# Optimization experiments

Measured on AMD Instinct MI355X. Metric: run time of the kernel, lower is better.

Reference implementation:

```python
import jax, jax.numpy as jnp
import numpy as np

B, SQ, SK = 32, 512, 512
Q_DIM = 512
K_DIM = 512
H = 8
HD = 64
INNER = H * HD
MAX_POS = 512
SCALE = 1.0 / np.sqrt(HD)


def setup_inputs() -> dict:
    key = jax.random.key(0)
    ks = jax.random.split(key, 10)
    query = jax.random.normal(ks[0], (B, SQ, Q_DIM), dtype=jnp.float32)
    key_t = jax.random.normal(ks[1], (B, SK, K_DIM), dtype=jnp.float32)
    value = jax.random.normal(ks[2], (B, SK, K_DIM), dtype=jnp.float32)
    mask = jax.random.randint(ks[3], (B, SQ, SK), 0, 2, dtype=jnp.int32)
    # learned parameters (Linear weights stored as [in, out]; to_q/k/v have no bias)
    Wq = jax.random.normal(ks[4], (Q_DIM, INNER), dtype=jnp.float32) * 0.02
    Wk = jax.random.normal(ks[5], (K_DIM, INNER), dtype=jnp.float32) * 0.02
    Wv = jax.random.normal(ks[6], (K_DIM, INNER), dtype=jnp.float32) * 0.02
    Wo = jax.random.normal(ks[7], (INNER, Q_DIM), dtype=jnp.float32) * 0.02
    bo = jnp.zeros((Q_DIM,), dtype=jnp.float32)
    rel_pos_emb = jax.random.normal(ks[8], (MAX_POS, MAX_POS), dtype=jnp.float32) * 0.02
    return {"query": query, "key": key_t, "value": value, "mask": mask,
            "Wq": Wq, "Wk": Wk, "Wv": Wv, "Wo": Wo, "bo": bo,
            "rel_pos_emb": rel_pos_emb}


def reference(query, key, value, mask, Wq, Wk, Wv, Wo, bo, rel_pos_emb):
    # Projections (no bias for q/k/v)
    q = query @ Wq   # [B, SQ, INNER]
    k = key @ Wk     # [B, SK, INNER]
    v = value @ Wv   # [B, SK, INNER]
    # split heads -> [B, H, S, HD]
    q = q.reshape(B, SQ, H, HD).transpose(0, 2, 1, 3)
    k = k.reshape(B, SK, H, HD).transpose(0, 2, 1, 3)
    v = v.reshape(B, SK, H, HD).transpose(0, 2, 1, 3)
    # scaled scores + learned relative-position bias (shared across batch/heads)
    scores = jnp.einsum('bhqd,bhkd->bhqk', q, k) * SCALE
    bias = rel_pos_emb[:SQ, :SK]          # [SQ, SK]
    scores = scores + bias[None, None, :, :]
    # additive masking: positions where mask == 0 get -inf
    scores = jnp.where(mask[:, None, :, :] == 0, -jnp.inf, scores)
    attn = jax.nn.softmax(scores, axis=-1)
    # dropout is identity in eval mode (p treated as inference)
    out = jnp.einsum('bhqk,bhkd->bhqd', attn, v)
    out = out.transpose(0, 2, 1, 3).reshape(B, SQ, INNER)
    return out @ Wo + bo
```

## Files before the change

### kernel.cpp

```cpp
#include <hip/hip_runtime.h>
#include <stdint.h>


typedef unsigned short u16;
typedef __attribute__((ext_vector_type(4))) float f32x4;
typedef __attribute__((ext_vector_type(8))) __bf16 bf16x8;
typedef __attribute__((ext_vector_type(4))) unsigned short u16x4;
typedef __attribute__((ext_vector_type(8))) unsigned short u16x8;
typedef __attribute__((ext_vector_type(4))) int i32x4;
typedef __attribute__((ext_vector_type(4))) _Float16 f16x4;
typedef __attribute__((ext_vector_type(8))) _Float16 f16x8;

#define MFMA16(a, b, c) __builtin_amdgcn_mfma_f32_16x16x32_bf16((a), (b), (c), 0, 0, 0)

#define LGKM0_BARRIER()                                        \
  do {                                                         \
    asm volatile("s_waitcnt lgkmcnt(0)" ::: "memory");         \
    __builtin_amdgcn_s_barrier();                              \
    __builtin_amdgcn_sched_barrier(0);                         \
  } while (0)

__device__ __forceinline__ u16 f2bf(float f) {
  unsigned u = __float_as_uint(f);
  u += 0x7fffu + ((u >> 16) & 1u);
  return (u16)(u >> 16);
}
__device__ __forceinline__ float bf2f(u16 h) {
  return __uint_as_float(((unsigned)h) << 16);
}

__device__ __forceinline__ void gl_lds16(const void* g, void* l) {
  __builtin_amdgcn_global_load_lds(
      (const __attribute__((address_space(1))) unsigned int*)g,
      (__attribute__((address_space(3))) unsigned int*)l, 16, 0, 0);
}

__global__ __launch_bounds__(256) void k_prep(
    const float* __restrict__ Wq, const float* __restrict__ Wk,
    const float* __restrict__ Wv, const float* __restrict__ Wo,
    u16* __restrict__ Wt, u16* __restrict__ WoHi, u16* __restrict__ WoLo) {
  int idx = blockIdx.x * 256 + threadIdx.x;
  int n = idx >> 9, k = idx & 511;
  int src = k * 512 + n;
  Wt[idx]          = f2bf(Wq[src]);
  Wt[262144 + idx] = f2bf(Wk[src]);
  Wt[524288 + idx] = f2bf(Wv[src]);
  float wo = Wo[src];
  u16 hi = f2bf(wo);
  WoHi[idx] = hi;
  WoLo[idx] = f2bf(wo - bf2f(hi));
}

__global__ __launch_bounds__(256) void k_cvt(
    const float* __restrict__ Xq, const float* __restrict__ Xk,
    const float* __restrict__ Xv, u16* __restrict__ Xb) {
  const float* __restrict__ src =
      (blockIdx.y == 0) ? Xq : (blockIdx.y == 1) ? Xk : Xv;
  size_t i8 = ((size_t)blockIdx.x * 256 + threadIdx.x) * 8;
  f32x4 v0 = *(const f32x4*)&src[i8];
  f32x4 v1 = *(const f32x4*)&src[i8 + 4];
  u16x8 o;
#pragma unroll
  for (int e = 0; e < 4; ++e) {
    o[e]     = f2bf(v0[e]);
    o[e + 4] = f2bf(v1[e]);
  }
  *(u16x8*)&Xb[(size_t)blockIdx.y * 8388608 + i8] = o;
}

__global__ __launch_bounds__(256) void k_mb(
    const int* __restrict__ mask, const float* __restrict__ bias,
    _Float16* __restrict__ MB) {
  size_t i8 = ((size_t)blockIdx.x * 256 + threadIdx.x) * 8;
  i32x4 m0 = *(const i32x4*)&mask[i8];
  i32x4 m1 = *(const i32x4*)&mask[i8 + 4];
  size_t bi = i8 & 262143;
  f32x4 b0 = *(const f32x4*)&bias[bi];
  f32x4 b1 = *(const f32x4*)&bias[bi + 4];
  const _Float16 MASKED = (_Float16)(-60000.0f);
  f16x8 o;
#pragma unroll
  for (int e = 0; e < 4; ++e) {
    o[e]     = (m0[e] != 0) ? (_Float16)b0[e] : MASKED;
    o[e + 4] = (m1[e] != 0) ? (_Float16)b1[e] : MASKED;
  }
  *(f16x8*)&MB[i8] = o;
}

__global__ __launch_bounds__(512, 4) void k_proj(
    const u16* __restrict__ Xb, const u16* __restrict__ Wt,
    u16* __restrict__ Qb, u16* __restrict__ Kb, u16* __restrict__ Vtb) {
  __shared__ __align__(16) u16 lAb[2][128][64];
  const int mat = blockIdx.z;
  const u16* __restrict__ Ab = Xb + (size_t)mat * 8388608;
  const u16* __restrict__ Bw = Wt + (size_t)mat * 262144;
  const int tid = threadIdx.x, lane = tid & 63, wid = tid >> 6;
  const int wm = wid >> 2, wn = wid & 3;
  const int m0 = blockIdx.y * 128, n0 = blockIdx.x * 256;
  const int fr = lane & 15, g = lane >> 4;

  const int sub = lane >> 3;
  const int xo = ((lane & 7) ^ sub) * 8;
  const int swr = (fr & 7) << 4;

  const u16* __restrict__ Bp[4];
#pragma unroll
  for (int fn = 0; fn < 4; ++fn)
    Bp[fn] = &Bw[(size_t)(n0 + wn * 64 + fn * 16 + fr) * 512 + g * 8];

  f32x4 acc[4][4] = {};

#pragma unroll
  for (int p = 0; p < 2; ++p) {
    const int rb = p * 64 + wid * 8;
    gl_lds16(Ab + (size_t)(m0 + rb + sub) * 512 + xo, &lAb[0][rb][0]);
  }
  __syncthreads();

  for (int kt = 0; kt < 8; ++kt) {
    const int cur = kt & 1, nxt = cur ^ 1;
    const int k0 = kt * 64;
    bf16x8 bB[2][4];
#pragma unroll
    for (int fn = 0; fn < 4; ++fn) {
      bB[0][fn] = *(const bf16x8*)(Bp[fn] + k0);
      bB[1][fn] = *(const bf16x8*)(Bp[fn] + k0 + 32);
    }
    if (kt < 7) {
#pragma unroll
      for (int p = 0; p < 2; ++p) {
        const int rb = p * 64 + wid * 8;
        gl_lds16(Ab + (size_t)(m0 + rb + sub) * 512 + k0 + 64 + xo,
                 &lAb[nxt][rb][0]);
      }
    }
#pragma unroll
    for (int kc = 0; kc < 2; ++kc) {
#pragma unroll
      for (int fm = 0; fm < 4; ++fm) {
        const char* rowb = (const char*)&lAb[cur][wm * 64 + fm * 16 + fr][0];
        bf16x8 af = *(const bf16x8*)(rowb + ((kc * 64 + g * 16) ^ swr));
#pragma unroll
        for (int fn = 0; fn < 4; ++fn)
          acc[fm][fn] = MFMA16(af, bB[kc][fn], acc[fm][fn]);
      }
    }
    __syncthreads();
  }

  if (mat < 2) {
    u16* __restrict__ Out = (mat == 0) ? Qb : Kb;
#pragma unroll
    for (int fm = 0; fm < 4; ++fm) {
#pragma unroll
      for (int fn = 0; fn < 4; ++fn) {
        int gn = n0 + wn * 64 + fn * 16 + fr;
        int hh = gn >> 6, hd = gn & 63;
#pragma unroll
        for (int r = 0; r < 4; ++r) {
          int gm = m0 + wm * 64 + fm * 16 + g * 4 + r;
          int b = gm >> 9, sq = gm & 511;
          Out[(size_t)((b * 8 + hh) * 512 + sq) * 64 + hd] = f2bf(acc[fm][fn][r]);
        }
      }
    }
  } else {
#pragma unroll
    for (int fm = 0; fm < 4; ++fm) {
      int gm0 = m0 + wm * 64 + fm * 16 + g * 4;
      int b = gm0 >> 9, sq0 = gm0 & 511;
#pragma unroll
      for (int fn = 0; fn < 4; ++fn) {
        int gn = n0 + wn * 64 + fn * 16 + fr;
        int hh = gn >> 6, hd = gn & 63;
        u16x4 pv;
        pv[0] = f2bf(acc[fm][fn][0]); pv[1] = f2bf(acc[fm][fn][1]);
        pv[2] = f2bf(acc[fm][fn][2]); pv[3] = f2bf(acc[fm][fn][3]);
        *(u16x4*)&Vtb[(size_t)((b * 8 + hh) * 64 + hd) * 512 + sq0] = pv;
      }
    }
  }
}

__global__ __launch_bounds__(256, 4) void k_attn(
    const u16* __restrict__ Qb, const u16* __restrict__ Kb, const u16* __restrict__ Vtb,
    const _Float16* __restrict__ MB, float* __restrict__ Obuf) {
  __shared__ __align__(16) u16 kbuf[2][64][64];
  __shared__ __align__(16) u16 vbuf[2][64][64];
  __shared__ __align__(16) u16 lP[4][16][64];
  const int tid = threadIdx.x, lane = tid & 63, w = tid >> 6;
  const int orig = blockIdx.x;
  const int xcd = orig & 7, idx = orig >> 3;
  const int qq = idx & 3, h = (idx >> 2) & 7;
  const int b = xcd + 8 * (idx >> 5);
  const int bh = b * 8 + h;
  const int fr = lane & 15, g = lane >> 4;
  const int sq0 = qq * 128 + w * 32;
  const int sw = (fr & 7) << 4;
  const u16* __restrict__ Qh = Qb + (size_t)bh * 32768;
  const u16* __restrict__ Kh = Kb + (size_t)bh * 32768;
  const u16* __restrict__ Vh = Vtb + (size_t)bh * 32768;
  const _Float16* __restrict__ MBr = MB + (size_t)b * 262144 + (size_t)(sq0 + fr) * 512;
  char* lProw = (char*)&lP[w][fr][0];
  const char* kcb;
  const char* vcb;

  const int sub = lane >> 3;
  const int xo = ((lane & 7) ^ sub) * 8;

  bf16x8 qf[2][2];
#pragma unroll
  for (int qfi = 0; qfi < 2; ++qfi)
#pragma unroll
    for (int kc = 0; kc < 2; ++kc)
      qf[qfi][kc] = *(const bf16x8*)&Qh[(size_t)(sq0 + qfi * 16 + fr) * 64 + kc * 32 + g * 8];

  f32x4 oacc[2][4] = {};
  float mrow[2] = {-1e30f, -1e30f}, lrow[2] = {0.f, 0.f};

  {
    if (w < 2) {
      const int rb = w * 32;
      const u16* gs = Kh + (size_t)(rb + sub) * 64 + xo;
#pragma unroll
      for (int i = 0; i < 4; ++i)
        gl_lds16(gs + (size_t)i * 8 * 64, &kbuf[0][rb + i * 8][0]);
    } else {
      const int rb = (w - 2) * 32;
      const u16* gs = Vh + (size_t)(rb + sub) * 512 + xo;
#pragma unroll
      for (int i = 0; i < 4; ++i)
        gl_lds16(gs + (size_t)i * 8 * 512, &vbuf[0][rb + i * 8][0]);
    }
  }
  __syncthreads();

  int cur = 0;
  for (int kt = 0; kt < 8; ++kt) {
    const int sk0 = kt * 64;
    f16x4 mbv[2][4];
#pragma unroll
    for (int qfi = 0; qfi < 2; ++qfi)
#pragma unroll
      for (int fn = 0; fn < 4; ++fn)
        mbv[qfi][fn] = *(const f16x4*)&MBr[(size_t)qfi * 16 * 512 + sk0 + fn * 16 + g * 4];
    if (kt < 7) {
      const int nb = cur ^ 1, sk0n = sk0 + 64;
      if (w < 2) {
        const int rb = w * 32;
        const u16* gs = Kh + (size_t)(sk0n + rb + sub) * 64 + xo;
#pragma unroll
        for (int i = 0; i < 4; ++i)
          gl_lds16(gs + (size_t)i * 8 * 64, &kbuf[nb][rb + i * 8][0]);
      } else {
        const int rb = (w - 2) * 32;
        const u16* gs = Vh + (size_t)(rb + sub) * 512 + sk0n + xo;
#pragma unroll
        for (int i = 0; i < 4; ++i)
          gl_lds16(gs + (size_t)i * 8 * 512, &vbuf[nb][rb + i * 8][0]);
      }
    }
    kcb = (const char*)kbuf[cur];
    vcb = (const char*)vbuf[cur];
    f32x4 sacc[2][4] = {};
#pragma unroll
    for (int fn = 0; fn < 4; ++fn) {
      const int r = fn * 16 + fr;
      bf16x8 kf0 = *(const bf16x8*)(kcb + (size_t)r * 128 + ((0 * 64 + g * 16) ^ sw));
      bf16x8 kf1 = *(const bf16x8*)(kcb + (size_t)r * 128 + ((1 * 64 + g * 16) ^ sw));
      sacc[0][fn] = MFMA16(kf0, qf[0][0], sacc[0][fn]);
      sacc[0][fn] = MFMA16(kf1, qf[0][1], sacc[0][fn]);
      sacc[1][fn] = MFMA16(kf0, qf[1][0], sacc[1][fn]);
      sacc[1][fn] = MFMA16(kf1, qf[1][1], sacc[1][fn]);
    }
#pragma unroll
    for (int qfi = 0; qfi < 2; ++qfi)
#pragma unroll
      for (int fn = 0; fn < 4; ++fn)
#pragma unroll
        for (int r = 0; r < 4; ++r)
          sacc[qfi][fn][r] = sacc[qfi][fn][r] * 0.125f + (float)mbv[qfi][fn][r];

#pragma unroll
    for (int qfi = 0; qfi < 2; ++qfi) {
      float t0 = fmaxf(fmaxf(sacc[qfi][0][0], sacc[qfi][0][1]),
                       fmaxf(sacc[qfi][0][2], sacc[qfi][0][3]));
      float t1 = fmaxf(fmaxf(sacc[qfi][1][0], sacc[qfi][1][1]),
                       fmaxf(sacc[qfi][1][2], sacc[qfi][1][3]));
      float t2 = fmaxf(fmaxf(sacc[qfi][2][0], sacc[qfi][2][1]),
                       fmaxf(sacc[qfi][2][2], sacc[qfi][2][3]));
      float t3 = fmaxf(fmaxf(sacc[qfi][3][0], sacc[qfi][3][1]),
                       fmaxf(sacc[qfi][3][2], sacc[qfi][3][3]));
      float pm = fmaxf(fmaxf(t0, t1), fmaxf(t2, t3));
      pm = fmaxf(pm, __shfl_xor(pm, 16));
      pm = fmaxf(pm, __shfl_xor(pm, 32));
      if (!__all(pm - mrow[qfi] <= 8.0f)) {
        float mn = fmaxf(mrow[qfi], pm);
        float sfac = __expf(mrow[qfi] - mn);
        mrow[qfi] = mn;
        lrow[qfi] *= sfac;
#pragma unroll
        for (int r = 0; r < 4; ++r) {
          float sr = __shfl(sfac, g * 4 + r);
#pragma unroll
          for (int fnh = 0; fnh < 4; ++fnh)
            oacc[qfi][fnh][r] *= sr;
        }
      }
      float ps = 0.f;
#pragma unroll
      for (int fn = 0; fn < 4; ++fn) {
        float p0 = __expf(sacc[qfi][fn][0] - mrow[qfi]);
        float p1 = __expf(sacc[qfi][fn][1] - mrow[qfi]);
        float p2 = __expf(sacc[qfi][fn][2] - mrow[qfi]);
        float p3 = __expf(sacc[qfi][fn][3] - mrow[qfi]);
        ps += (p0 + p1) + (p2 + p3);
        u16x4 pw;
        pw[0] = f2bf(p0); pw[1] = f2bf(p1); pw[2] = f2bf(p2); pw[3] = f2bf(p3);
        *(u16x4*)(lProw + ((fn * 32 + g * 8) ^ sw)) = pw;
      }
      ps += __shfl_xor(ps, 16);
      ps += __shfl_xor(ps, 32);
      lrow[qfi] += ps;
      __builtin_amdgcn_wave_barrier();
#pragma unroll
      for (int kc = 0; kc < 2; ++kc) {
        bf16x8 pf = *(const bf16x8*)(lProw + ((kc * 64 + g * 16) ^ sw));
#pragma unroll
        for (int fnh = 0; fnh < 4; ++fnh) {
          const int vr = fnh * 16 + fr;
          bf16x8 vf = *(const bf16x8*)(vcb + (size_t)vr * 128 + ((kc * 64 + g * 16) ^ sw));
          oacc[qfi][fnh] = MFMA16(pf, vf, oacc[qfi][fnh]);
        }
      }
      __builtin_amdgcn_wave_barrier();
    }
    __syncthreads();
    cur ^= 1;
  }
#pragma unroll
  for (int qfi = 0; qfi < 2; ++qfi) {
#pragma unroll
    for (int r = 0; r < 4; ++r) {
      float lr = __shfl(lrow[qfi], g * 4 + r);
      float inv = 1.0f / lr;
      const int sq = sq0 + qfi * 16 + g * 4 + r;
      float* orow = &Obuf[((size_t)b * 512 + sq) * 512 + h * 64];
#pragma unroll
      for (int fnh = 0; fnh < 4; ++fnh)
        orow[fnh * 16 + fr] = oacc[qfi][fnh][r] * inv;
    }
  }
}

__global__ __launch_bounds__(512, 4) void k_out(
    const float* __restrict__ Oin, const u16* __restrict__ WoHi, const u16* __restrict__ WoLo,
    const float* __restrict__ bo, float* __restrict__ out) {
  __shared__ __align__(16) u16 lAh[2][64][40], lAl[2][64][40];
  const int tid = threadIdx.x, lane = tid & 63, wn = tid >> 6;
  const int m0 = blockIdx.y * 64, n0 = blockIdx.x * 256;
  const int fr = lane & 15, g = lane >> 4;
  const int arow = tid >> 3, acg = tid & 7;
  const float* __restrict__ Ar = &Oin[(size_t)(m0 + arow) * 512 + acg * 4];
  const u16* __restrict__ Bh[2];
  const u16* __restrict__ Bl[2];
#pragma unroll
  for (int fn = 0; fn < 2; ++fn) {
    size_t row = (size_t)(n0 + wn * 32 + fn * 16 + fr) * 512 + g * 8;
    Bh[fn] = &WoHi[row];
    Bl[fn] = &WoLo[row];
  }

  f32x4 acc[4][2] = {};
  f32x4 va[2];

  {
    f32x4 v = *(const f32x4*)&Ar[0];
    va[0] = *(const f32x4*)&Ar[32];
    u16x4 hv, lv;
#pragma unroll
    for (int e = 0; e < 4; ++e) {
      u16 hb = f2bf(v[e]);
      hv[e] = hb;
      lv[e] = f2bf(v[e] - bf2f(hb));
    }
    *(u16x4*)&lAh[0][arow][acg * 4] = hv;
    *(u16x4*)&lAl[0][arow][acg * 4] = lv;
  }
  LGKM0_BARRIER();

#pragma unroll
  for (int kt = 0; kt < 16; ++kt) {
    const int cur = kt & 1, nxt = cur ^ 1;
    const int k0 = kt * 32;
    bf16x8 bh[2], bl[2];
#pragma unroll
    for (int fn = 0; fn < 2; ++fn) {
      bh[fn] = *(const bf16x8*)(Bh[fn] + k0);
      bl[fn] = *(const bf16x8*)(Bl[fn] + k0);
    }
    if (kt < 14)
      va[nxt] = *(const f32x4*)&Ar[(kt + 2) * 32];
#pragma unroll
    for (int fm = 0; fm < 4; ++fm) {
      bf16x8 ah = *(const bf16x8*)&lAh[cur][fm * 16 + fr][g * 8];
      bf16x8 al = *(const bf16x8*)&lAl[cur][fm * 16 + fr][g * 8];
#pragma unroll
      for (int fn = 0; fn < 2; ++fn) {
        acc[fm][fn] = MFMA16(ah, bh[fn], acc[fm][fn]);
        acc[fm][fn] = MFMA16(ah, bl[fn], acc[fm][fn]);
        acc[fm][fn] = MFMA16(al, bh[fn], acc[fm][fn]);
      }
    }
    if (kt < 15) {
      u16x4 hv, lv;
#pragma unroll
      for (int e = 0; e < 4; ++e) {
        u16 hb = f2bf(va[cur][e]);
        hv[e] = hb;
        lv[e] = f2bf(va[cur][e] - bf2f(hb));
      }
      *(u16x4*)&lAh[nxt][arow][acg * 4] = hv;
      *(u16x4*)&lAl[nxt][arow][acg * 4] = lv;
    }
    LGKM0_BARRIER();
  }

#pragma unroll
  for (int fm = 0; fm < 4; ++fm) {
#pragma unroll
    for (int fn = 0; fn < 2; ++fn) {
      int gn = n0 + wn * 32 + fn * 16 + fr;
      float bv = bo[gn];
#pragma unroll
      for (int r = 0; r < 4; ++r) {
        int gm = m0 + fm * 16 + g * 4 + r;
        out[(size_t)gm * 512 + gn] = acc[fm][fn][r] + bv;
      }
    }
  }
}

extern "C" void kernel_launch(void* const* d_in, const int* in_sizes, int n_in,
                              void* d_out, int out_size, void* d_ws, size_t ws_size,
                              hipStream_t stream) {
  (void)in_sizes; (void)n_in; (void)out_size; (void)ws_size;
  const float* query = (const float*)d_in[0];
  const float* key_t = (const float*)d_in[1];
  const float* value = (const float*)d_in[2];
  const int*   mask  = (const int*)d_in[3];
  const float* Wq    = (const float*)d_in[4];
  const float* Wk    = (const float*)d_in[5];
  const float* Wv    = (const float*)d_in[6];
  const float* Wo    = (const float*)d_in[7];
  const float* bo    = (const float*)d_in[8];
  const float* bias  = (const float*)d_in[9];
  float* out = (float*)d_out;

  char* p = (char*)d_ws;
  u16* Wt   = (u16*)p; p += (size_t)3 * 512 * 512 * 2;
  u16* WoHi = (u16*)p; p += (size_t)512 * 512 * 2;
  u16* WoLo = (u16*)p; p += (size_t)512 * 512 * 2;
  u16* Qb   = (u16*)p; p += (size_t)32 * 8 * 512 * 64 * 2;
  u16* Kb   = (u16*)p; p += (size_t)32 * 8 * 512 * 64 * 2;
  u16* Vtb  = (u16*)p; p += (size_t)32 * 8 * 512 * 64 * 2;
  u16* Xb = (u16*)p;
  float* Obuf = (float*)p;
  _Float16* MBp = (_Float16*)(p + (size_t)32 * 512 * 512 * 4);

  k_prep<<<1024, 256, 0, stream>>>(Wq, Wk, Wv, Wo, Wt, WoHi, WoLo);
  k_cvt<<<dim3(4096, 3), 256, 0, stream>>>(query, key_t, value, Xb);
  k_proj<<<dim3(2, 128, 3), 512, 0, stream>>>(Xb, Wt, Qb, Kb, Vtb);
  k_mb<<<4096, 256, 0, stream>>>(mask, bias, MBp);
  k_attn<<<1024, 256, 0, stream>>>(Qb, Kb, Vtb, MBp, Obuf);
  k_out<<<dim3(2, 256), 512, 0, stream>>>(Obuf, WoHi, WoLo, bo, out);
}
```

Measured before the change: 194.3 us.

## Pre-swizzle weights into MFMA fragment order and shrink proj/out blocks to 256 threads

The weight prep kernel now writes Wq/Wk/Wv and the Wo hi/lo split in MFMA B-fragment order. Each wave can then load its B operand as one fully contiguous 1KB chunk per k-step instead of strided row reads. k_proj and k_out are reshaped to 256-thread blocks covering 128 output columns, with twice as many blocks launched and A-tile loading adjusted to match. This targets uncoalesced weight loads and aims at better occupancy, at the cost of reloading A tiles across more column blocks.

```diff
diff --git a/kernel.cpp b/kernel.cpp
--- a/kernel.cpp
+++ b/kernel.cpp
@@ -39,16 +39,32 @@
     const float* __restrict__ Wq, const float* __restrict__ Wk,
     const float* __restrict__ Wv, const float* __restrict__ Wo,
     u16* __restrict__ Wt, u16* __restrict__ WoHi, u16* __restrict__ WoLo) {
-  int idx = blockIdx.x * 256 + threadIdx.x;
-  int n = idx >> 9, k = idx & 511;
-  int src = k * 512 + n;
-  Wt[idx]          = f2bf(Wq[src]);
-  Wt[262144 + idx] = f2bf(Wk[src]);
-  Wt[524288 + idx] = f2bf(Wv[src]);
-  float wo = Wo[src];
-  u16 hi = f2bf(wo);
-  WoHi[idx] = hi;
-  WoLo[idx] = f2bf(wo - bf2f(hi));
+  int t = blockIdx.x * 256 + threadIdx.x;
+  int mat = t >> 15;
+  int r = t & 32767;
+  int nc = r >> 10, kb = (r >> 6) & 15, lane = r & 63;
+  int fr = lane & 15, g = lane >> 4;
+  int n = nc * 16 + fr;
+  int kbase = kb * 32 + g * 8;
+  if (mat < 3) {
+    const float* __restrict__ W = (mat == 0) ? Wq : (mat == 1) ? Wk : Wv;
+    u16x8 o;
+#pragma unroll
+    for (int j = 0; j < 8; ++j)
+      o[j] = f2bf(W[(size_t)(kbase + j) * 512 + n]);
+    *(u16x8*)&Wt[(size_t)mat * 262144 + (size_t)r * 8] = o;
+  } else {
+    u16x8 oh, ol;
+#pragma unroll
+    for (int j = 0; j < 8; ++j) {
+      float wo = Wo[(size_t)(kbase + j) * 512 + n];
+      u16 hi = f2bf(wo);
+      oh[j] = hi;
+      ol[j] = f2bf(wo - bf2f(hi));
+    }
+    *(u16x8*)&WoHi[(size_t)r * 8] = oh;
+    *(u16x8*)&WoLo[(size_t)r * 8] = ol;
+  }
 }
 
 __global__ __launch_bounds__(256) void k_cvt(
@@ -87,32 +103,33 @@
   *(f16x8*)&MB[i8] = o;
 }
 
-__global__ __launch_bounds__(512, 4) void k_proj(
+__global__ __launch_bounds__(256, 4) void k_proj(
     const u16* __restrict__ Xb, const u16* __restrict__ Wt,
     u16* __restrict__ Qb, u16* __restrict__ Kb, u16* __restrict__ Vtb) {
   __shared__ __align__(16) u16 lAb[2][128][64];
   const int mat = blockIdx.z;
   const u16* __restrict__ Ab = Xb + (size_t)mat * 8388608;
-  const u16* __restrict__ Bw = Wt + (size_t)mat * 262144;
+  const u16* __restrict__ Bf = Wt + (size_t)mat * 262144;
   const int tid = threadIdx.x, lane = tid & 63, wid = tid >> 6;
-  const int wm = wid >> 2, wn = wid & 3;
-  const int m0 = blockIdx.y * 128, n0 = blockIdx.x * 256;
+  const int wm = wid >> 1, wn = wid & 1;
+  const int m0 = blockIdx.y * 128, n0 = blockIdx.x * 128;
   const int fr = lane & 15, g = lane >> 4;
 
   const int sub = lane >> 3;
   const int xo = ((lane & 7) ^ sub) * 8;
   const int swr = (fr & 7) << 4;
 
-  const u16* __restrict__ Bp[4];
+  const int nc0 = (n0 >> 4) + wn * 4;
+  const u16* __restrict__ Bq[4];
 #pragma unroll
   for (int fn = 0; fn < 4; ++fn)
-    Bp[fn] = &Bw[(size_t)(n0 + wn * 64 + fn * 16 + fr) * 512 + g * 8];
+    Bq[fn] = Bf + (size_t)((nc0 + fn) * 16) * 512 + lane * 8;
 
   f32x4 acc[4][4] = {};
 
 #pragma unroll
-  for (int p = 0; p < 2; ++p) {
-    const int rb = p * 64 + wid * 8;
+  for (int p = 0; p < 4; ++p) {
+    const int rb = p * 32 + wid * 8;
     gl_lds16(Ab + (size_t)(m0 + rb + sub) * 512 + xo, &lAb[0][rb][0]);
   }
   __syncthreads();
@@ -123,13 +140,13 @@
     bf16x8 bB[2][4];
 #pragma unroll
     for (int fn = 0; fn < 4; ++fn) {
-      bB[0][fn] = *(const bf16x8*)(Bp[fn] + k0);
-      bB[1][fn] = *(const bf16x8*)(Bp[fn] + k0 + 32);
+      bB[0][fn] = *(const bf16x8*)(Bq[fn] + (size_t)(kt * 2) * 512);
+      bB[1][fn] = *(const bf16x8*)(Bq[fn] + (size_t)(kt * 2 + 1) * 512);
     }
     if (kt < 7) {
 #pragma unroll
-      for (int p = 0; p < 2; ++p) {
-        const int rb = p * 64 + wid * 8;
+      for (int p = 0; p < 4; ++p) {
+        const int rb = p * 32 + wid * 8;
         gl_lds16(Ab + (size_t)(m0 + rb + sub) * 512 + k0 + 64 + xo,
                  &lAb[nxt][rb][0]);
       }
@@ -353,54 +370,60 @@
   }
 }
 
-__global__ __launch_bounds__(512, 4) void k_out(
+__global__ __launch_bounds__(256, 4) void k_out(
     const float* __restrict__ Oin, const u16* __restrict__ WoHi, const u16* __restrict__ WoLo,
     const float* __restrict__ bo, float* __restrict__ out) {
   __shared__ __align__(16) u16 lAh[2][64][40], lAl[2][64][40];
   const int tid = threadIdx.x, lane = tid & 63, wn = tid >> 6;
-  const int m0 = blockIdx.y * 64, n0 = blockIdx.x * 256;
+  const int m0 = blockIdx.y * 64, n0 = blockIdx.x * 128;
   const int fr = lane & 15, g = lane >> 4;
-  const int arow = tid >> 3, acg = tid & 7;
-  const float* __restrict__ Ar = &Oin[(size_t)(m0 + arow) * 512 + acg * 4];
-  const u16* __restrict__ Bh[2];
-  const u16* __restrict__ Bl[2];
+  const int arow = tid >> 2, acg = tid & 3;
+  const float* __restrict__ Ar = &Oin[(size_t)(m0 + arow) * 512 + acg * 8];
+  const int nc0 = (n0 >> 4) + wn * 2;
+  const u16* __restrict__ Bhp[2];
+  const u16* __restrict__ Blp[2];
 #pragma unroll
   for (int fn = 0; fn < 2; ++fn) {
-    size_t row = (size_t)(n0 + wn * 32 + fn * 16 + fr) * 512 + g * 8;
-    Bh[fn] = &WoHi[row];
-    Bl[fn] = &WoLo[row];
+    size_t off = (size_t)((nc0 + fn) * 16) * 512 + lane * 8;
+    Bhp[fn] = WoHi + off;
+    Blp[fn] = WoLo + off;
   }
 
   f32x4 acc[4][2] = {};
-  f32x4 va[2];
+  f32x4 va[2][2];
 
   {
-    f32x4 v = *(const f32x4*)&Ar[0];
-    va[0] = *(const f32x4*)&Ar[32];
-    u16x4 hv, lv;
+    f32x4 v0 = *(const f32x4*)&Ar[0];
+    f32x4 v1 = *(const f32x4*)&Ar[4];
+    va[0][0] = *(const f32x4*)&Ar[32];
+    va[0][1] = *(const f32x4*)&Ar[36];
+    u16x8 hv, lv;
 #pragma unroll
     for (int e = 0; e < 4; ++e) {
-      u16 hb = f2bf(v[e]);
-      hv[e] = hb;
-      lv[e] = f2bf(v[e] - bf2f(hb));
-    }
-    *(u16x4*)&lAh[0][arow][acg * 4] = hv;
-    *(u16x4*)&lAl[0][arow][acg * 4] = lv;
+      u16 hb0 = f2bf(v0[e]);
+      u16 hb1 = f2bf(v1[e]);
+      hv[e] = hb0; hv[e + 4] = hb1;
+      lv[e] = f2bf(v0[e] - bf2f(hb0));
+      lv[e + 4] = f2bf(v1[e] - bf2f(hb1));
+    }
+    *(u16x8*)&lAh[0][arow][acg * 8] = hv;
+    *(u16x8*)&lAl[0][arow][acg * 8] = lv;
   }
   LGKM0_BARRIER();
 
 #pragma unroll
   for (int kt = 0; kt < 16; ++kt) {
     const int cur = kt & 1, nxt = cur ^ 1;
-    const int k0 = kt * 32;
     bf16x8 bh[2], bl[2];
 #pragma unroll
     for (int fn = 0; fn < 2; ++fn) {
-      bh[fn] = *(const bf16x8*)(Bh[fn] + k0);
-      bl[fn] = *(const bf16x8*)(Bl[fn] + k0);
-    }
-    if (kt < 14)
-      va[nxt] = *(const f32x4*)&Ar[(kt + 2) * 32];
+      bh[fn] = *(const bf16x8*)(Bhp[fn] + (size_t)kt * 512);
+      bl[fn] = *(const bf16x8*)(Blp[fn] + (size_t)kt * 512);
+    }
+    if (kt < 14) {
+      va[nxt][0] = *(const f32x4*)&Ar[(kt + 2) * 32];
+      va[nxt][1] = *(const f32x4*)&Ar[(kt + 2) * 32 + 4];
+    }
 #pragma unroll
     for (int fm = 0; fm < 4; ++fm) {
       bf16x8 ah = *(const bf16x8*)&lAh[cur][fm * 16 + fr][g * 8];
@@ -413,15 +436,17 @@
       }
     }
     if (kt < 15) {
-      u16x4 hv, lv;
+      u16x8 hv, lv;
 #pragma unroll
       for (int e = 0; e < 4; ++e) {
-        u16 hb = f2bf(va[cur][e]);
-        hv[e] = hb;
-        lv[e] = f2bf(va[cur][e] - bf2f(hb));
-      }
-      *(u16x4*)&lAh[nxt][arow][acg * 4] = hv;
-      *(u16x4*)&lAl[nxt][arow][acg * 4] = lv;
+        u16 hb0 = f2bf(va[cur][0][e]);
+        u16 hb1 = f2bf(va[cur][1][e]);
+        hv[e] = hb0; hv[e + 4] = hb1;
+        lv[e] = f2bf(va[cur][0][e] - bf2f(hb0));
+        lv[e + 4] = f2bf(va[cur][1][e] - bf2f(hb1));
+      }
+      *(u16x8*)&lAh[nxt][arow][acg * 8] = hv;
+      *(u16x8*)&lAl[nxt][arow][acg * 8] = lv;
     }
     LGKM0_BARRIER();
   }
@@ -468,10 +493,10 @@
   float* Obuf = (float*)p;
   _Float16* MBp = (_Float16*)(p + (size_t)32 * 512 * 512 * 4);
 
-  k_prep<<<1024, 256, 0, stream>>>(Wq, Wk, Wv, Wo, Wt, WoHi, WoLo);
+  k_prep<<<512, 256, 0, stream>>>(Wq, Wk, Wv, Wo, Wt, WoHi, WoLo);
   k_cvt<<<dim3(4096, 3), 256, 0, stream>>>(query, key_t, value, Xb);
-  k_proj<<<dim3(2, 128, 3), 512, 0, stream>>>(Xb, Wt, Qb, Kb, Vtb);
+  k_proj<<<dim3(4, 128, 3), 256, 0, stream>>>(Xb, Wt, Qb, Kb, Vtb);
   k_mb<<<4096, 256, 0, stream>>>(mask, bias, MBp);
   k_attn<<<1024, 256, 0, stream>>>(Qb, Kb, Vtb, MBp, Obuf);
-  k_out<<<dim3(2, 256), 512, 0, stream>>>(Obuf, WoHi, WoLo, bo, out);
-}
+  k_out<<<dim3(4, 256), 256, 0, stream>>>(Obuf, WoHi, WoLo, bo, out);
+}
```

Measured after the change: 182.4 us. -6.1%, faster.
